# Kernel tuning notes

Hardware: AMD Instinct MI355X
Metric: run time of the kernel (lower is better)

## Reference

```python
import jax, jax.numpy as jnp
import numpy as np

IN_DIM = 128
LAYER_DIMS = [128, 128]
NUM_SAMPLES = [25, 10]
L0 = 3072
NEG_WEIGHT = 1.0


def setup_inputs() -> dict:
    key = jax.random.key(0)
    ks = jax.random.split(key, 12)
    feat = jax.random.normal(ks[0], (L0, IN_DIM), dtype=jnp.float32)
    nodes = jax.random.randint(ks[1], (L0,), 0, L0)
    nb0 = jnp.arange(L0)
    nb1 = jax.random.randint(ks[2], (L0 * 10,), 0, L0)
    nb2 = jax.random.randint(ks[3], (L0 * 10 * 25,), 0, L0)
    src_idx = jax.random.randint(ks[4], (1024,), 0, L0)
    pos_idx = jax.random.randint(ks[5], (1024,), 0, L0)
    neg_idx = jax.random.randint(ks[6], (512,), 0, L0)
    g = 0.05
    # mean aggregator weights: layer0 in=IN_DIM, layer1 in=2*128 (concat)
    w_self_0 = jax.random.normal(ks[7], (IN_DIM, 128), jnp.float32) * g
    w_neigh_0 = jax.random.normal(ks[8], (IN_DIM, 128), jnp.float32) * g
    w_self_1 = jax.random.normal(ks[9], (256, 128), jnp.float32) * g
    w_neigh_1 = jax.random.normal(ks[10], (256, 128), jnp.float32) * g
    return dict(nodes=nodes, feat=feat, src_idx=src_idx, pos_idx=pos_idx,
                neg_idx=neg_idx, nb0=nb0, nb1=nb1, nb2=nb2,
                w_self_0=w_self_0, w_neigh_0=w_neigh_0,
                w_self_1=w_self_1, w_neigh_1=w_neigh_1)


def _aggregate(hidden, params):
    # GraphSAGE layer stack: at layer l, combine each hop with the mean of its
    # sampled neighbors, concat self/neigh transforms, relu except last layer.
    num_layers = len(NUM_SAMPLES)
    for layer in range(num_layers):
        w_self, w_neigh = params[layer]
        is_last = layer == num_layers - 1
        next_hidden = []
        for hop in range(num_layers - layer):
            s = NUM_SAMPLES[num_layers - hop - 1]
            self_v = hidden[hop]  # [n, d]
            neigh = hidden[hop + 1].reshape(self_v.shape[0], s, self_v.shape[1])
            neigh_mean = jnp.mean(neigh, axis=1)
            h = jnp.concatenate([self_v @ w_self, neigh_mean @ w_neigh], axis=1)
            if not is_last:
                h = jax.nn.relu(h)
            next_hidden.append(h)
        hidden = next_hidden
    return hidden[0]


def _l2_normalize(x, eps=1e-12):
    return x * jax.lax.rsqrt(jnp.maximum(jnp.sum(x * x, axis=1, keepdims=True), eps))


def reference(nodes, feat, src_idx, pos_idx, neg_idx, nb0, nb1, nb2,
              w_self_0, w_neigh_0, w_self_1, w_neigh_1):
    hidden = [feat[nb0], feat[nb1], feat[nb2]]
    params = [(w_self_0, w_neigh_0), (w_self_1, w_neigh_1)]
    output = _aggregate(hidden, params)          # [L0, 256]
    output = _l2_normalize(output)
    src_emb = output[src_idx]                    # [B, 256]
    pos_emb = output[pos_idx]
    neg_emb = output[neg_idx]                    # [Nneg, 256]

    aff = jnp.sum(src_emb * pos_emb, axis=1)     # [B]
    neg_aff = src_emb @ neg_emb.T                # [B, Nneg]

    # MRR via double argsort (tf double top_k equivalent; ties -> positive last)
    aff_all = jnp.concatenate([neg_aff, aff[:, None]], axis=1)
    order = jnp.argsort(-aff_all, axis=1, stable=True)
    ranks = jnp.argsort(order, axis=1, stable=True)
    mrr = jnp.mean(1.0 / (ranks[:, -1].astype(jnp.float32) + 1.0))

    # sigmoid cross-entropy: labels 1 -> softplus(-x); labels 0 -> softplus(x)
    true_xent = jax.nn.softplus(-aff)
    neg_xent = jax.nn.softplus(neg_aff)
    loss = jnp.sum(true_xent) + NEG_WEIGHT * jnp.sum(neg_xent)
    loss = loss / jnp.asarray(src_emb.shape[0], jnp.float32)
    return src_emb, loss, mrr
```

## Files before the change

kernel.cpp:

```cpp
#include <hip/hip_runtime.h>
#include <math.h>

#define L0      3072
#define BATCH   1024
#define NNEG    512


__device__ __forceinline__ float bf2f(unsigned short u) {
  return __uint_as_float(((unsigned)u) << 16);
}
__device__ __forceinline__ void store_out(float v, float* p) { *p = v; }
__device__ __forceinline__ void store_out(float v, unsigned short* p) {
  unsigned x = __float_as_uint(v);
  *p = (unsigned short)((x + 0x7fff + ((x >> 16) & 1)) >> 16);
}

template<int K, int AW, int HOFF, bool NORM, typename OutT>
__global__ __launch_bounds__(512) void k_mm(
    const float* __restrict__ Ain,
    const float* __restrict__ W0, const float* __restrict__ W1,
    OutT* __restrict__ Out, const int ldo, const int outHalfOff) {
  __shared__ float AT[6 * AW];
  __shared__ float rs[8][3];
  const int t = threadIdx.x;
  const int base = blockIdx.x * 6;
  {
    const float4* __restrict__ src = (const float4*)(Ain + base * AW);
    float4* __restrict__ dst = (float4*)AT;
    for (int idx = t; idx < 6 * AW / 4; idx += 512) dst[idx] = src[idx];
  }
  __syncthreads();

  const int wave = t >> 6;
  const int half = wave >> 2;
  const int colg = (wave >> 1) & 1;
  const int rowg = wave & 1;
  const int rg = rowg * 3;
  const int col = colg * 64 + (t & 63);
  const float* __restrict__ W = (half ? W1 : W0) + col;
  const float* __restrict__ A0 = AT + rg * AW + half * HOFF;

  float acc[3] = {0.f, 0.f, 0.f};
#pragma unroll 4
  for (int d = 0; d < K; d += 4) {
    float4 a[3];
#pragma unroll
    for (int r = 0; r < 3; ++r) a[r] = *(const float4*)&A0[r * AW + d];
    float w[4];
#pragma unroll
    for (int i2 = 0; i2 < 4; ++i2) w[i2] = W[(d + i2) * 128];
#pragma unroll
    for (int i2 = 0; i2 < 4; ++i2)
#pragma unroll
      for (int r = 0; r < 3; ++r)
        acc[r] = fmaf(((const float*)&a[r])[i2], w[i2], acc[r]);
  }

  float scale[3] = {1.f, 1.f, 1.f};
  if (NORM) {
    float p[3];
#pragma unroll
    for (int r = 0; r < 3; ++r) p[r] = acc[r] * acc[r];
#pragma unroll
    for (int off = 32; off > 0; off >>= 1)
#pragma unroll
      for (int r = 0; r < 3; ++r) p[r] += __shfl_xor(p[r], off, 64);
    if ((t & 63) == 0) { rs[wave][0] = p[0]; rs[wave][1] = p[1]; rs[wave][2] = p[2]; }
    __syncthreads();
#pragma unroll
    for (int r = 0; r < 3; ++r) {
      const float s = rs[rowg][r] + rs[rowg + 2][r] + rs[rowg + 4][r] + rs[rowg + 6][r];
      scale[r] = rsqrtf(fmaxf(s, 1e-12f));
    }
  }
  OutT* __restrict__ O = Out + half * outHalfOff;
#pragma unroll
  for (int r = 0; r < 3; ++r)
    store_out(acc[r] * scale[r], &O[(base + rg + r) * ldo + col]);
}

__global__ __launch_bounds__(640) void k_aggregate(
    const unsigned short* __restrict__ X0, const unsigned short* __restrict__ Y0,
    const int* __restrict__ nb0, const int* __restrict__ nb1,
    const int* __restrict__ nb2, float* __restrict__ H) {
  __shared__ float gB[10][128], gC[10][128], gD[10][128];
  const int i = blockIdx.x;
  const int t = threadIdx.x;
  const int n0 = nb0[i];
  const int j = t >> 6;
  const int lam = t & 63;
  const int r = i * 10 + j;
  int myidx = 0;
  if (lam < 25) myidx = nb2[r * 25 + lam];
  else if (lam == 25) myidx = nb1[r];
  const int c8 = lam & 15;
  const int sub = lam >> 4;

  float d8[8];
#pragma unroll
  for (int e = 0; e < 8; ++e) d8[e] = 0.f;
#pragma unroll
  for (int m = 0; m < 7; ++m) {
    const int k = sub + 4 * m;
    const int ridx = __shfl(myidx, k, 64);
    if (k < 25) {
      const float4 raw = *(const float4*)(Y0 + ridx * 128 + c8 * 8);
      const unsigned short* u = (const unsigned short*)&raw;
#pragma unroll
      for (int e = 0; e < 8; ++e) d8[e] += bf2f(u[e]);
    }
  }
#pragma unroll
  for (int e = 0; e < 8; ++e) d8[e] += __shfl_xor(d8[e], 16, 64);
#pragma unroll
  for (int e = 0; e < 8; ++e) d8[e] += __shfl_xor(d8[e], 32, 64);

  const int r1 = __shfl(myidx, 25, 64);
  if (sub == 0) {
#pragma unroll
    for (int e = 0; e < 8; ++e) gD[j][c8 * 8 + e] = fmaxf(d8[e] * 0.04f, 0.f);
    const float4 raw = *(const float4*)(Y0 + r1 * 128 + c8 * 8);
    const unsigned short* u = (const unsigned short*)&raw;
#pragma unroll
    for (int e = 0; e < 8; ++e) gB[j][c8 * 8 + e] = bf2f(u[e]);
  } else if (sub == 1) {
    const float4 raw = *(const float4*)(X0 + r1 * 128 + c8 * 8);
    const unsigned short* u = (const unsigned short*)&raw;
#pragma unroll
    for (int e = 0; e < 8; ++e) gC[j][c8 * 8 + e] = fmaxf(bf2f(u[e]), 0.f);
  }
  __syncthreads();

  if (t < 512) {
    const int q = t >> 7, c = t & 127;
    float v;
    if (q == 0) {
      v = fmaxf(bf2f(X0[n0 * 128 + c]), 0.f);
    } else {
      const float* g = (q == 1) ? &gB[0][0] : (q == 2) ? &gC[0][0] : &gD[0][0];
      float s = 0.f;
#pragma unroll
      for (int jj = 0; jj < 10; ++jj) s += g[jj * 128 + c];
      v = s * 0.1f;
      if (q == 1) v = fmaxf(v, 0.f);
    }
    H[i * 512 + t] = v;
  }
}

__device__ __forceinline__ float softplusf(float x) {
  return fmaxf(x, 0.f) + log1pf(expf(-fabsf(x)));
}

__global__ __launch_bounds__(256) void k_prep(
    const float* __restrict__ R, const int* __restrict__ neg_idx,
    float* __restrict__ NT) {
  const int p = blockIdx.x;
  const int t = threadIdx.x;
  const int c = (p & 7) * 64 + (t & 63);
  const int d4 = (p >> 3) * 4 + (t >> 6);
  const float4 v = *(const float4*)&R[neg_idx[c] * 256 + d4 * 4];
#pragma unroll
  for (int i2 = 0; i2 < 4; ++i2)
    NT[(d4 * 4 + i2) * 512 + c] = ((const float*)&v)[i2];
}

__global__ __launch_bounds__(256) void k_neg(
    const float* __restrict__ O, const float* __restrict__ NT,
    const int* __restrict__ src_idx, const int* __restrict__ pos_idx,
    float* __restrict__ out_src, int* __restrict__ rankPart,
    float* __restrict__ spPosPart, float* __restrict__ spNegPart) {
  __shared__ float SP[32 * 260];
  __shared__ float affL[16];
  __shared__ int cntL[16];
  __shared__ float wsum[8];
  const int t = threadIdx.x;
  const int bid = blockIdx.x;
  const int rowBase = (bid >> 3) * 16;
  const int colBase = (bid & 7) * 64;
  const bool first = (colBase == 0);

  {
    const float4* __restrict__ s4 = (const float4*)O;
#pragma unroll
    for (int idx = t; idx < 32 * 64; idx += 256) {
      const int row = idx >> 6, c4 = idx & 63;
      const int rid = (row < 16) ? src_idx[rowBase + row]
                                 : pos_idx[rowBase + row - 16];
      *(float4*)&SP[row * 260 + c4 * 4] = s4[rid * 64 + c4];
    }
  }
  if (first) {
    const float4* __restrict__ s4 = (const float4*)O;
    float4* __restrict__ d4o = (float4*)out_src;
#pragma unroll
    for (int idx = t; idx < 16 * 64; idx += 256) {
      const int rr = idx >> 6, c4 = idx & 63;
      d4o[(rowBase + rr) * 64 + c4] = s4[src_idx[rowBase + rr] * 64 + c4];
    }
  }
  __syncthreads();

  const int tc = t & 31;
  const int rowg = t >> 5;
  const float* __restrict__ B = NT + colBase + 2 * tc;
  const float* __restrict__ A0 = SP + rowg * 260;
  const float* __restrict__ A1 = SP + (rowg + 8) * 260;
  const float* __restrict__ SV = SP + t * 260;
  const float* __restrict__ PV = SP + (16 + t) * 260;

  float acc00 = 0.f, acc01 = 0.f, acc10 = 0.f, acc11 = 0.f, aff = 0.f;
#pragma unroll 4
  for (int d4 = 0; d4 < 64; ++d4) {
    const int dd = d4 * 4;
    const float4 a0 = *(const float4*)&A0[dd];
    const float4 a1 = *(const float4*)&A1[dd];
    float2 b[4];
#pragma unroll
    for (int i2 = 0; i2 < 4; ++i2)
      b[i2] = *(const float2*)&B[(dd + i2) * 512];
    float4 sv, pv;
    if (t < 16) {
      sv = *(const float4*)&SV[dd];
      pv = *(const float4*)&PV[dd];
    }
#pragma unroll
    for (int i2 = 0; i2 < 4; ++i2) {
      const float va0 = ((const float*)&a0)[i2];
      const float va1 = ((const float*)&a1)[i2];
      acc00 = fmaf(va0, b[i2].x, acc00);
      acc01 = fmaf(va0, b[i2].y, acc01);
      acc10 = fmaf(va1, b[i2].x, acc10);
      acc11 = fmaf(va1, b[i2].y, acc11);
      if (t < 16)
        aff = fmaf(((const float*)&sv)[i2], ((const float*)&pv)[i2], aff);
    }
  }
  if (t < 16) affL[t] = aff;
  __syncthreads();

  float sp = softplusf(acc00) + softplusf(acc01) +
             softplusf(acc10) + softplusf(acc11);
  const float av0 = affL[rowg], av1 = affL[rowg + 8];
  int c0 = ((acc00 >= av0) ? 1 : 0) + ((acc01 >= av0) ? 1 : 0);
  int c1 = ((acc10 >= av1) ? 1 : 0) + ((acc11 >= av1) ? 1 : 0);
#pragma unroll
  for (int off = 16; off > 0; off >>= 1) {
    sp += __shfl_down(sp, off, 32);
    c0 += __shfl_down(c0, off, 32);
    c1 += __shfl_down(c1, off, 32);
  }
  if ((t & 31) == 0) {
    cntL[rowg] = c0;
    cntL[rowg + 8] = c1;
    wsum[rowg] = sp;
  }
  __syncthreads();

  if (t < 16) rankPart[(bid & 7) * 1024 + rowBase + t] = cntL[t];
  if (t == 0)
    spNegPart[bid] = wsum[0] + wsum[1] + wsum[2] + wsum[3] +
                     wsum[4] + wsum[5] + wsum[6] + wsum[7];
  if (first && t == 0) {
    float ps = 0.f;
#pragma unroll
    for (int r = 0; r < 16; ++r) ps += softplusf(-affL[r]);
    spPosPart[bid >> 3] = ps;
  }
}

__global__ __launch_bounds__(256) void k_finalize(
    const int* __restrict__ rankPart, const float* __restrict__ spPosPart,
    const float* __restrict__ spNegPart, float* __restrict__ out) {
  __shared__ float wa[4], wb[4];
  const int t = threadIdx.x;
  float s = 0.f;
  for (int i = t; i < BATCH; i += 256) {
    int rv = 0;
#pragma unroll
    for (int p = 0; p < 8; ++p) rv += rankPart[p * 1024 + i];
    s += 1.f / (float)(rv + 1);
  }
  float l = 0.f;
  for (int i = t; i < 512; i += 256) l += spNegPart[i];
  if (t < 64) l += spPosPart[t];
#pragma unroll
  for (int off = 32; off > 0; off >>= 1) {
    s += __shfl_down(s, off, 64);
    l += __shfl_down(l, off, 64);
  }
  if ((t & 63) == 0) { wa[t >> 6] = s; wb[t >> 6] = l; }
  __syncthreads();
  if (t == 0) {
    out[BATCH * 256]     = (wb[0] + wb[1] + wb[2] + wb[3]) * (1.f / 1024.f);
    out[BATCH * 256 + 1] = (wa[0] + wa[1] + wa[2] + wa[3]) * (1.f / 1024.f);
  }
}

extern "C" void kernel_launch(void* const* d_in, const int* in_sizes, int n_in,
                              void* d_out, int out_size, void* d_ws, size_t ws_size,
                              hipStream_t stream) {
  const float* feat   = (const float*)d_in[1];
  const int* src_idx  = (const int*)d_in[2];
  const int* pos_idx  = (const int*)d_in[3];
  const int* neg_idx  = (const int*)d_in[4];
  const int* nb0      = (const int*)d_in[5];
  const int* nb1      = (const int*)d_in[6];
  const int* nb2      = (const int*)d_in[7];
  const float* ws0    = (const float*)d_in[8];
  const float* wn0    = (const float*)d_in[9];
  const float* ws1    = (const float*)d_in[10];
  const float* wn1    = (const float*)d_in[11];

  float* wsf = (float*)d_ws;
  unsigned short* X0 = (unsigned short*)d_ws;
  unsigned short* Y0 = X0 + 393216;
  float* H       = wsf + 393216;
  float* R       = wsf + 1966080;
  float* spPosP  = wsf + 2752512;
  float* spNegP  = wsf + 2752640;
  int*   rankP   = (int*)(wsf + 2753664);
  float* NT      = wsf + 2761856;
  float* out     = (float*)d_out;

  k_mm<128, 128, 0, false, unsigned short><<<L0 / 6, 512, 0, stream>>>(
      feat, ws0, wn0, X0, 128, 393216);
  k_aggregate<<<L0, 640, 0, stream>>>(X0, Y0, nb0, nb1, nb2, H);
  k_mm<256, 512, 256, true, float><<<L0 / 6, 512, 0, stream>>>(
      H, ws1, wn1, R, 256, 128);
  k_prep<<<128, 256, 0, stream>>>(R, neg_idx, NT);
  k_neg<<<512, 256, 0, stream>>>(
      R, NT, src_idx, pos_idx, out, rankP, spPosP, spNegP);
  k_finalize<<<1, 256, 0, stream>>>(rankP, spPosP, spNegP, out);
}
```

Measured before the change: 161.0 us.

## Fuse negative-embedding transpose into k_neg with LDS staging and larger row tiles

Result: faster. 157.7 us (-2.1%).

```diff
diff --git a/kernel.cpp b/kernel.cpp
--- a/kernel.cpp
+++ b/kernel.cpp
@@ -152,49 +152,50 @@
   return fmaxf(x, 0.f) + log1pf(expf(-fabsf(x)));
 }
 
-__global__ __launch_bounds__(256) void k_prep(
-    const float* __restrict__ R, const int* __restrict__ neg_idx,
-    float* __restrict__ NT) {
-  const int p = blockIdx.x;
-  const int t = threadIdx.x;
-  const int c = (p & 7) * 64 + (t & 63);
-  const int d4 = (p >> 3) * 4 + (t >> 6);
-  const float4 v = *(const float4*)&R[neg_idx[c] * 256 + d4 * 4];
-#pragma unroll
-  for (int i2 = 0; i2 < 4; ++i2)
-    NT[(d4 * 4 + i2) * 512 + c] = ((const float*)&v)[i2];
-}
-
-__global__ __launch_bounds__(256) void k_neg(
-    const float* __restrict__ O, const float* __restrict__ NT,
+__global__ __launch_bounds__(512) void k_neg(
+    const float* __restrict__ O,
     const int* __restrict__ src_idx, const int* __restrict__ pos_idx,
+    const int* __restrict__ neg_idx,
     float* __restrict__ out_src, int* __restrict__ rankPart,
     float* __restrict__ spPosPart, float* __restrict__ spNegPart) {
-  __shared__ float SP[32 * 260];
-  __shared__ float affL[16];
-  __shared__ int cntL[16];
-  __shared__ float wsum[8];
+  __shared__ float SP[64 * 260];
+  __shared__ float BT[256 * 64];
+  __shared__ float affL[32];
+  __shared__ int cntL[32];
+  __shared__ float wsum[16];
   const int t = threadIdx.x;
   const int bid = blockIdx.x;
-  const int rowBase = (bid >> 3) * 16;
+  const int rowBase = (bid >> 3) * 32;
   const int colBase = (bid & 7) * 64;
-  const bool first = (colBase == 0);
+  const bool first = ((bid & 7) == 0);
 
   {
     const float4* __restrict__ s4 = (const float4*)O;
 #pragma unroll
-    for (int idx = t; idx < 32 * 64; idx += 256) {
+    for (int idx = t; idx < 64 * 64; idx += 512) {
       const int row = idx >> 6, c4 = idx & 63;
-      const int rid = (row < 16) ? src_idx[rowBase + row]
-                                 : pos_idx[rowBase + row - 16];
+      const int rid = (row < 32) ? src_idx[rowBase + row]
+                                 : pos_idx[rowBase + row - 32];
       *(float4*)&SP[row * 260 + c4 * 4] = s4[rid * 64 + c4];
+    }
+  }
+  {
+    const float4* __restrict__ s4 = (const float4*)O;
+#pragma unroll
+    for (int idx = t; idx < 64 * 64; idx += 512) {
+      const int j = idx & 63, c4 = idx >> 6;
+      const float4 v = s4[neg_idx[colBase + j] * 64 + c4];
+      BT[(4 * c4 + 0) * 64 + j] = v.x;
+      BT[(4 * c4 + 1) * 64 + j] = v.y;
+      BT[(4 * c4 + 2) * 64 + j] = v.z;
+      BT[(4 * c4 + 3) * 64 + j] = v.w;
     }
   }
   if (first) {
     const float4* __restrict__ s4 = (const float4*)O;
     float4* __restrict__ d4o = (float4*)out_src;
 #pragma unroll
-    for (int idx = t; idx < 16 * 64; idx += 256) {
+    for (int idx = t; idx < 32 * 64; idx += 512) {
       const int rr = idx >> 6, c4 = idx & 63;
       d4o[(rowBase + rr) * 64 + c4] = s4[src_idx[rowBase + rr] * 64 + c4];
     }
@@ -203,11 +204,10 @@
 
   const int tc = t & 31;
   const int rowg = t >> 5;
-  const float* __restrict__ B = NT + colBase + 2 * tc;
   const float* __restrict__ A0 = SP + rowg * 260;
-  const float* __restrict__ A1 = SP + (rowg + 8) * 260;
+  const float* __restrict__ A1 = SP + (rowg + 16) * 260;
   const float* __restrict__ SV = SP + t * 260;
-  const float* __restrict__ PV = SP + (16 + t) * 260;
+  const float* __restrict__ PV = SP + (32 + t) * 260;
 
   float acc00 = 0.f, acc01 = 0.f, acc10 = 0.f, acc11 = 0.f, aff = 0.f;
 #pragma unroll 4
@@ -218,9 +218,9 @@
     float2 b[4];
 #pragma unroll
     for (int i2 = 0; i2 < 4; ++i2)
-      b[i2] = *(const float2*)&B[(dd + i2) * 512];
+      b[i2] = *(const float2*)&BT[(dd + i2) * 64 + 2 * tc];
     float4 sv, pv;
-    if (t < 16) {
+    if (t < 32) {
       sv = *(const float4*)&SV[dd];
       pv = *(const float4*)&PV[dd];
     }
@@ -232,16 +232,16 @@
       acc01 = fmaf(va0, b[i2].y, acc01);
       acc10 = fmaf(va1, b[i2].x, acc10);
       acc11 = fmaf(va1, b[i2].y, acc11);
-      if (t < 16)
+      if (t < 32)
         aff = fmaf(((const float*)&sv)[i2], ((const float*)&pv)[i2], aff);
     }
   }
-  if (t < 16) affL[t] = aff;
+  if (t < 32) affL[t] = aff;
   __syncthreads();
 
   float sp = softplusf(acc00) + softplusf(acc01) +
              softplusf(acc10) + softplusf(acc11);
-  const float av0 = affL[rowg], av1 = affL[rowg + 8];
+  const float av0 = affL[rowg], av1 = affL[rowg + 16];
   int c0 = ((acc00 >= av0) ? 1 : 0) + ((acc01 >= av0) ? 1 : 0);
   int c1 = ((acc10 >= av1) ? 1 : 0) + ((acc11 >= av1) ? 1 : 0);
 #pragma unroll
@@ -252,19 +252,22 @@
   }
   if ((t & 31) == 0) {
     cntL[rowg] = c0;
-    cntL[rowg + 8] = c1;
+    cntL[rowg + 16] = c1;
     wsum[rowg] = sp;
   }
   __syncthreads();
 
-  if (t < 16) rankPart[(bid & 7) * 1024 + rowBase + t] = cntL[t];
-  if (t == 0)
-    spNegPart[bid] = wsum[0] + wsum[1] + wsum[2] + wsum[3] +
-                     wsum[4] + wsum[5] + wsum[6] + wsum[7];
+  if (t < 32) rankPart[(bid & 7) * 1024 + rowBase + t] = cntL[t];
+  if (t == 0) {
+    float sn = 0.f;
+#pragma unroll
+    for (int w = 0; w < 16; ++w) sn += wsum[w];
+    spNegPart[bid] = sn;
+  }
   if (first && t == 0) {
     float ps = 0.f;
 #pragma unroll
-    for (int r = 0; r < 16; ++r) ps += softplusf(-affL[r]);
+    for (int r = 0; r < 32; ++r) ps += softplusf(-affL[r]);
     spPosPart[bid >> 3] = ps;
   }
 }
@@ -282,8 +285,8 @@
     s += 1.f / (float)(rv + 1);
   }
   float l = 0.f;
-  for (int i = t; i < 512; i += 256) l += spNegPart[i];
-  if (t < 64) l += spPosPart[t];
+  if (t < 256) l += spNegPart[t];
+  if (t < 32) l += spPosPart[t];
 #pragma unroll
   for (int off = 32; off > 0; off >>= 1) {
     s += __shfl_down(s, off, 64);
@@ -320,7 +323,6 @@
   float* spPosP  = wsf + 2752512;
   float* spNegP  = wsf + 2752640;
   int*   rankP   = (int*)(wsf + 2753664);
-  float* NT      = wsf + 2761856;
   float* out     = (float*)d_out;
 
   k_mm<128, 128, 0, false, unsigned short><<<L0 / 6, 512, 0, stream>>>(
@@ -328,8 +330,7 @@
   k_aggregate<<<L0, 640, 0, stream>>>(X0, Y0, nb0, nb1, nb2, H);
   k_mm<256, 512, 256, true, float><<<L0 / 6, 512, 0, stream>>>(
       H, ws1, wn1, R, 256, 128);
-  k_prep<<<128, 256, 0, stream>>>(R, neg_idx, NT);
-  k_neg<<<512, 256, 0, stream>>>(
-      R, NT, src_idx, pos_idx, out, rankP, spPosP, spNegP);
+  k_neg<<<256, 512, 0, stream>>>(
+      R, src_idx, pos_idx, neg_idx, out, rankP, spPosP, spNegP);
   k_finalize<<<1, 256, 0, stream>>>(rankP, spPosP, spNegP, out);
 }
```
